# Kernel optimization log

Measured on AMD Instinct MI355X. Metric: run time of the kernel, lower is better.

The kernel has to match this reference:

```python
import jax, jax.numpy as jnp
import numpy as np

NEG = -1e12


def setup_inputs() -> dict:
    key = jax.random.key(0)
    ks = jax.random.split(key, 10)
    B, C, Q, D = 16, 384, 64, 2048
    return {
        "c": jax.random.normal(ks[0], (B, C, D), dtype=jnp.float32),
        "q": jax.random.normal(ks[1], (B, Q, D), dtype=jnp.float32),
        "c_len": jax.random.randint(ks[2], (B,), 1, C + 1),
        "q_len": jax.random.randint(ks[3], (B,), 1, Q + 1),
        "w_c": jax.random.normal(ks[4], (D,), dtype=jnp.float32) * 0.02,
        "b_c": jnp.zeros((), dtype=jnp.float32),
        "w_q": jax.random.normal(ks[5], (D,), dtype=jnp.float32) * 0.02,
        "b_q": jnp.zeros((), dtype=jnp.float32),
        "w_cq": jax.random.normal(ks[6], (D,), dtype=jnp.float32) * 0.02,
        "b_cq": jnp.zeros((), dtype=jnp.float32),
        "W_out": jax.random.normal(ks[7], (4 * D, 2), dtype=jnp.float32) * 0.02,
        "b_out": jnp.zeros((2,), dtype=jnp.float32),
    }


def reference(c, q, c_len, q_len, w_c, b_c, w_q, b_q, w_cq, b_cq, W_out, b_out):
    B, C, D = c.shape
    Q = q.shape[1]
    # trilinear similarity: s[b,r,i] = w_c.c_r + w_q.q_i + w_cq.(c_r*q_i) + biases
    cq = jnp.einsum('bcd,bqd,d->bcq', c, q, w_cq) + b_cq          # [B,C,Q]
    s = (c @ w_c + b_c)[:, :, None] + (q @ w_q + b_q)[:, None, :] + cq
    rows = jnp.arange(C)[None, :, None]
    cols = jnp.arange(Q)[None, None, :]
    # faithful to the triple loop: cols >= q_len OR (rows >= c_len AND col < Q-1)
    masked = (cols >= q_len[:, None, None]) | (
        (rows >= c_len[:, None, None]) & (cols < Q - 1))
    s = s + jnp.where(masked, jnp.float32(NEG), jnp.float32(0.0))
    a = jax.nn.softmax(s, axis=2)                                  # [B,C,Q]
    c2q = jnp.einsum('bcq,bqd->bcd', a, q)                         # [B,C,D]
    b_att = jax.nn.softmax(jnp.max(s, axis=2), axis=1)             # [B,C]
    q2c = jnp.einsum('bc,bcd->bd', b_att, c)[:, None, :]           # [B,1,D]
    x = jnp.concatenate(
        [c, c2q, c * c2q, c * jnp.broadcast_to(q2c, c.shape)], axis=-1)
    out = x @ W_out + b_out                                        # [B,C,2]
    # final masking: out[i][c_len[i]:-1] = NEG (last row untouched)
    row_mask = (jnp.arange(C)[None, :] >= c_len[:, None]) & (
        jnp.arange(C)[None, :] < C - 1)
    out = jnp.where(row_mask[..., None], jnp.float32(NEG), out)
    return out[..., 0], out[..., 1]
```

## Files before the change

### kernel.cpp

```cpp
#include <hip/hip_runtime.h>

#define NEGV -1.0e12f
constexpr int B = 16, C = 384, Q = 64, D = 2048;
constexpr int PITCH = 40;
constexpr int IST = 8320;
constexpr int NIMG = 64;
constexpr int NT = 96;
constexpr int KC = 4;
constexpr int SP = 208;

typedef __attribute__((ext_vector_type(8))) short s16x8;
typedef __attribute__((ext_vector_type(4))) float f32x4;

__device__ __forceinline__ unsigned pkbf(float lo, float hi) {
  unsigned ulo = __builtin_bit_cast(unsigned, lo);
  unsigned uhi = __builtin_bit_cast(unsigned, hi);
  return (uhi & 0xFFFF0000u) | (ulo >> 16);
}
__device__ __forceinline__ float bflo(unsigned u) {
  return __builtin_bit_cast(float, u << 16);
}
__device__ __forceinline__ float bfhi(unsigned u) {
  return __builtin_bit_cast(float, u & 0xFFFF0000u);
}

#define GLD_LDS(gsrc, ldst)                                              \
  __builtin_amdgcn_global_load_lds(                                      \
      (const __attribute__((address_space(1))) unsigned*)(gsrc),         \
      (__attribute__((address_space(3))) unsigned*)(ldst), 16, 0, 0)

__global__ __launch_bounds__(256) void k_pq(
    const float* __restrict__ q, const float* __restrict__ w_cq,
    const float* __restrict__ w_c, const float* __restrict__ w_q,
    const float* __restrict__ W_out, unsigned short* __restrict__ bpk,
    float* __restrict__ qstats) {
  const int t = threadIdx.x;
  if (blockIdx.x < 512) {
    const int s = blockIdx.x & 31, b = blockIdx.x >> 5;
    const int k0 = s * 64;
    unsigned short* base = bpk + (size_t)b * NIMG * IST;
#pragma unroll
    for (int i = 0; i < 4; ++i) {
      int idx = t + 256 * i;
      int qi = idx >> 4, kc = (idx & 15) * 4;
      unsigned short* img = base + (size_t)(s * 2 + (kc >> 5)) * IST;
      const int ko = kc & 31;
      float4 qv = *(const float4*)(q + ((size_t)b * Q + qi) * D + k0 + kc);
      float4 wq = *(const float4*)(w_cq + k0 + kc);
      const float* wp = W_out + (size_t)(2 * D + k0 + kc) * 2;
      float4 wa = *(const float4*)(wp);
      float4 wb = *(const float4*)(wp + 4);
      uint2 u;
      u.x = pkbf(qv.x * wq.x, qv.y * wq.y);
      u.y = pkbf(qv.z * wq.z, qv.w * wq.w);
      *(uint2*)(img + qi * PITCH + ko) = u;
      u.x = pkbf(qv.x * wa.x, qv.y * wa.z);
      u.y = pkbf(qv.z * wb.x, qv.w * wb.z);
      *(uint2*)(img + (64 + qi) * PITCH + ko) = u;
      u.x = pkbf(qv.x * wa.y, qv.y * wa.w);
      u.y = pkbf(qv.z * wb.y, qv.w * wb.w);
      *(uint2*)(img + (128 + qi) * PITCH + ko) = u;
    }
    if (t < 48) {
      int r = t >> 4, kc = (t & 15) * 4;
      unsigned short* img = base + (size_t)(s * 2 + (kc >> 5)) * IST;
      const int ko = kc & 31;
      uint2 u;
      if (r == 0) {
        float4 w = *(const float4*)(w_c + k0 + kc);
        u.x = pkbf(w.x, w.y);
        u.y = pkbf(w.z, w.w);
      } else {
        const float* wp = W_out + (size_t)(k0 + kc) * 2 + (r - 1);
        u.x = pkbf(wp[0], wp[2]);
        u.y = pkbf(wp[4], wp[6]);
      }
      *(uint2*)(img + (192 + r) * PITCH + ko) = u;
    }
  } else {
    int bi = blockIdx.x - 512;
    const float* qrow = q + (size_t)bi * D;
    float a0 = 0.f, a1 = 0.f, a2 = 0.f;
    for (int d = t * 4; d < D; d += 256 * 4) {
      float4 qv = *(const float4*)(qrow + d);
      float4 wq = *(const float4*)(w_q + d);
      const float* wp = W_out + (size_t)(D + d) * 2;
      float4 wa = *(const float4*)(wp);
      float4 wb = *(const float4*)(wp + 4);
      a0 += qv.x * wq.x + qv.y * wq.y + qv.z * wq.z + qv.w * wq.w;
      a1 += qv.x * wa.x + qv.y * wa.z + qv.z * wb.x + qv.w * wb.z;
      a2 += qv.x * wa.y + qv.y * wa.w + qv.z * wb.y + qv.w * wb.w;
    }
    for (int m = 1; m < 64; m <<= 1) {
      a0 += __shfl_xor(a0, m, 64);
      a1 += __shfl_xor(a1, m, 64);
      a2 += __shfl_xor(a2, m, 64);
    }
    __shared__ float red[3][4];
    int w = t >> 6, lane = t & 63;
    if (lane == 0) { red[0][w] = a0; red[1][w] = a1; red[2][w] = a2; }
    __syncthreads();
    if (t == 0) {
      qstats[bi * 3 + 0] = red[0][0] + red[0][1] + red[0][2] + red[0][3];
      qstats[bi * 3 + 1] = red[1][0] + red[1][1] + red[1][2] + red[1][3];
      qstats[bi * 3 + 2] = red[2][0] + red[2][1] + red[2][2] + red[2][3];
    }
  }
}

__global__ __launch_bounds__(512, 2) void k_score(
    const unsigned short* __restrict__ bpk, const float* __restrict__ c,
    float* __restrict__ S3p, unsigned short* __restrict__ cbf) {
  const int t = threadIdx.x;
  const int lane = t & 63, wv = t >> 6;
  const int bid = blockIdx.x;
  const int b = bid & 15, kcb = (bid >> 4) & 3, n0 = (bid >> 6) * NT;
  const int lr = lane & 15, lg = lane >> 4;
  const int mg = wv >> 1, ng = wv & 1;

  __shared__ unsigned short sBp[2][IST];
  __shared__ unsigned short sCp[2][NT * PITCH];

  const unsigned short* gB = bpk + ((size_t)b * NIMG + kcb * 16) * IST;
  const float* cbase = c + ((size_t)b * C + n0) * D + kcb * 512;
  unsigned short* cbf_base = cbf + ((size_t)b * C + n0) * D + kcb * 512;

  f32x4 acc[4][3];
#pragma unroll
  for (int f = 0; f < 4; ++f)
#pragma unroll
    for (int g = 0; g < 3; ++g) acc[f][g] = f32x4{0.f, 0.f, 0.f, 0.f};

  auto stageB = [&](int buf, int s) {
    const char* src = (const char*)gB + (size_t)s * (IST * 2);
    char* dst = (char*)&sBp[buf][0];
    GLD_LDS(src + t * 16, dst + t * 16);
    GLD_LDS(src + 8192 + t * 16, dst + 8192 + t * 16);
    if (t < 16) GLD_LDS(src + 16384 + t * 16, dst + 16384 + t * 16);
  };
  auto loadC = [&](float4* r, int s) {
    const float* base = cbase + s * 32;
    if (wv < 4) {
      int g0 = wv * 128 + lane;
      r[0] = *(const float4*)(base + (size_t)(g0 >> 3) * D + (g0 & 7) * 4);
      int g1 = g0 + 64;
      r[1] = *(const float4*)(base + (size_t)(g1 >> 3) * D + (g1 & 7) * 4);
    } else {
      int g0 = 512 + (wv - 4) * 64 + lane;
      r[0] = *(const float4*)(base + (size_t)(g0 >> 3) * D + (g0 & 7) * 4);
    }
  };
  auto writeC = [&](int buf, const float4* r, int s) {
    unsigned short* cb = cbf_base + s * 32;
    if (wv < 4) {
      int g0 = wv * 128 + lane;
      uint2 u0 = {pkbf(r[0].x, r[0].y), pkbf(r[0].z, r[0].w)};
      *(uint2*)&sCp[buf][(g0 >> 3) * PITCH + (g0 & 7) * 4] = u0;
      *(uint2*)(cb + (size_t)(g0 >> 3) * D + (g0 & 7) * 4) = u0;
      int g1 = g0 + 64;
      uint2 u1 = {pkbf(r[1].x, r[1].y), pkbf(r[1].z, r[1].w)};
      *(uint2*)&sCp[buf][(g1 >> 3) * PITCH + (g1 & 7) * 4] = u1;
      *(uint2*)(cb + (size_t)(g1 >> 3) * D + (g1 & 7) * 4) = u1;
    } else {
      int g0 = 512 + (wv - 4) * 64 + lane;
      uint2 u0 = {pkbf(r[0].x, r[0].y), pkbf(r[0].z, r[0].w)};
      *(uint2*)&sCp[buf][(g0 >> 3) * PITCH + (g0 & 7) * 4] = u0;
      *(uint2*)(cb + (size_t)(g0 >> 3) * D + (g0 & 7) * 4) = u0;
    }
  };
  auto compute = [&](int buf) {
    s16x8 af[4], bf[3];
#pragma unroll
    for (int f = 0; f < 4; ++f)
      af[f] = *(const s16x8*)&sBp[buf][(mg * 64 + f * 16 + lr) * PITCH +
                                       lg * 8];
#pragma unroll
    for (int g = 0; g < 3; ++g)
      bf[g] = *(const s16x8*)&sCp[buf][((ng * 3 + g) * 16 + lr) * PITCH +
                                       lg * 8];
#pragma unroll
    for (int f = 0; f < 4; ++f)
#pragma unroll
      for (int g = 0; g < 3; ++g)
        acc[f][g] =
            __builtin_amdgcn_mfma_f32_16x16x32_bf16(af[f], bf[g], acc[f][g],
                                                    0, 0, 0);
  };

  const int nvm = (wv == 0) ? 5 : ((wv < 4) ? 4 : 3);

  float4 rc[2][2];
  stageB(0, 0);
  loadC(rc[0], 0);
  for (int s = 0; s < 16; ++s) {
    const int cur = s & 1;
    if (s + 1 < 16) {
      stageB(cur ^ 1, s + 1);
      loadC(rc[cur ^ 1], s + 1);
      if (nvm == 5)
        asm volatile("s_waitcnt vmcnt(5)" ::: "memory");
      else if (nvm == 4)
        asm volatile("s_waitcnt vmcnt(4)" ::: "memory");
      else
        asm volatile("s_waitcnt vmcnt(3)" ::: "memory");
    } else {
      asm volatile("s_waitcnt vmcnt(0)" ::: "memory");
    }
    writeC(cur, rc[cur], s);
    asm volatile("s_waitcnt lgkmcnt(0)" ::: "memory");
    __builtin_amdgcn_sched_barrier(0);
    __builtin_amdgcn_s_barrier();
    compute(cur);
    __builtin_amdgcn_s_barrier();
  }

  const size_t rowbase = ((size_t)kcb * B + b) * C;
#pragma unroll
  for (int f = 0; f < 4; ++f) {
    int mf = mg * 4 + f;
    if (mf < 13) {
#pragma unroll
      for (int g = 0; g < 3; ++g) {
        int n = n0 + (ng * 3 + g) * 16 + lr;
        float* p = S3p + (rowbase + n) * SP + mf * 16 + lg * 4;
        *(f32x4*)p = acc[f][g];
      }
    }
  }
}

__global__ __launch_bounds__(256) void k_soft(
    const float* __restrict__ S3p, const float* __restrict__ qstats,
    const int* __restrict__ c_len, const int* __restrict__ q_len,
    const float* __restrict__ b_c, const float* __restrict__ b_q,
    const float* __restrict__ b_cq, float* __restrict__ mrow,
    float* __restrict__ out12) {
  const int t = threadIdx.x, lane = t & 63;
  const int rg = blockIdx.x * 4 + (t >> 6);
  const int b = rg / C, r = rg % C;
  float s_cq = 0.f, sc = 0.f, w10 = 0.f, w11 = 0.f, t30 = 0.f, t31 = 0.f;
#pragma unroll
  for (int p = 0; p < KC; ++p) {
    const float* Sr = S3p + ((size_t)p * B * C + rg) * SP;
    s_cq += Sr[lane];
    sc += Sr[192];
    w10 += Sr[193];
    w11 += Sr[194];
    t30 += Sr[64 + lane];
    t31 += Sr[128 + lane];
  }
  const float qs0 = qstats[((b << 6) + lane) * 3 + 0];
  const float qs1 = qstats[((b << 6) + lane) * 3 + 1];
  const float qs2 = qstats[((b << 6) + lane) * 3 + 2];
  float s = s_cq + sc + qs0 + b_c[0] + b_q[0] + b_cq[0];
  const int cl = c_len[b], ql = q_len[b];
  bool masked = (lane >= ql) || ((r >= cl) && (lane < Q - 1));
  if (masked) s += NEGV;
  float mx = s;
  for (int m = 1; m < 64; m <<= 1) mx = fmaxf(mx, __shfl_xor(mx, m, 64));
  float e = __expf(s - mx);
  float den = e;
  for (int m = 1; m < 64; m <<= 1) den += __shfl_xor(den, m, 64);
  float a = e / den;
  float v0 = a * (qs1 + t30);
  float v1 = a * (qs2 + t31);
  for (int m = 1; m < 64; m <<= 1) {
    v0 += __shfl_xor(v0, m, 64);
    v1 += __shfl_xor(v1, m, 64);
  }
  if (lane == 0) {
    mrow[rg] = mx;
    out12[rg * 2 + 0] = w10 + v0;
    out12[rg * 2 + 1] = w11 + v1;
  }
}

__global__ __launch_bounds__(512) void k_q2cu(
    const unsigned short* __restrict__ cbf, const float* __restrict__ mrow,
    const float* __restrict__ W_out, float* __restrict__ uvec) {
  const int ch = blockIdx.x, b = blockIdx.y;
  const int t = threadIdx.x, lane = t & 63, wv = t >> 6;
  __shared__ float batt[C];
  __shared__ float rmx[8], rsm[8];
  __shared__ float redq0[8][64], redq1[8][64];

  float m = (t < C) ? mrow[b * C + t] : -3.0e38f;
  float mx = m;
  for (int o = 1; o < 64; o <<= 1) mx = fmaxf(mx, __shfl_xor(mx, o, 64));
  if (lane == 0) rmx[wv] = mx;
  __syncthreads();
  mx = rmx[0];
#pragma unroll
  for (int i = 1; i < 8; ++i) mx = fmaxf(mx, rmx[i]);
  float e = (t < C) ? __expf(m - mx) : 0.f;
  float sm = e;
  for (int o = 1; o < 64; o <<= 1) sm += __shfl_xor(sm, o, 64);
  if (lane == 0) rsm[wv] = sm;
  __syncthreads();
  sm = rsm[0] + rsm[1] + rsm[2] + rsm[3] + rsm[4] + rsm[5] + rsm[6] + rsm[7];
  if (t < C) batt[t] = e / sm;
  __syncthreads();

  const int d0 = ch * 128 + lane * 2;
  const unsigned short* p = cbf + ((size_t)b * C + wv * 8) * D + d0;
  float A0[8] = {0.f, 0.f, 0.f, 0.f, 0.f, 0.f, 0.f, 0.f};
  float A1[8] = {0.f, 0.f, 0.f, 0.f, 0.f, 0.f, 0.f, 0.f};
#pragma unroll
  for (int r0 = 0; r0 < 384; r0 += 64) {
    const unsigned short* pr = p + (size_t)r0 * D;
    const float* bt = &batt[r0 + wv * 8];
#pragma unroll
    for (int j = 0; j < 8; ++j) {
      unsigned cc = *(const unsigned*)(pr + (size_t)j * D);
      A0[j] += bt[j] * bflo(cc);
      A1[j] += bt[j] * bfhi(cc);
    }
  }
  float s0 = ((A0[0] + A0[1]) + (A0[2] + A0[3])) +
             ((A0[4] + A0[5]) + (A0[6] + A0[7]));
  float s1 = ((A1[0] + A1[1]) + (A1[2] + A1[3])) +
             ((A1[4] + A1[5]) + (A1[6] + A1[7]));
  redq0[wv][lane] = s0;
  redq1[wv][lane] = s1;
  __syncthreads();
  if (t < 64) {
    float q0 = 0.f, q1 = 0.f;
#pragma unroll
    for (int w = 0; w < 8; ++w) {
      q0 += redq0[w][t];
      q1 += redq1[w][t];
    }
    int dd = ch * 128 + t * 2;
    float4 w4 = *(const float4*)(W_out + (size_t)(3 * D + dd) * 2);
    float4 u = {q0 * w4.x, q0 * w4.y, q1 * w4.z, q1 * w4.w};
    *(float4*)(uvec + ((size_t)b * D + dd) * 2) = u;
  }
}

__global__ __launch_bounds__(512) void k_out(
    const unsigned short* __restrict__ cbf, const float* __restrict__ uvec,
    const float* __restrict__ out12, const float* __restrict__ b_out,
    const int* __restrict__ c_len, float* __restrict__ outp) {
  const int b = blockIdx.y, r0 = blockIdx.x * 8;
  const int t = threadIdx.x, lane = t & 63, wv = t >> 6;
  __shared__ float u_sh[2 * D];

  {
    const float* src = uvec + (size_t)b * D * 2 + t * 8;
    float4 v0 = *(const float4*)(src);
    float4 v1 = *(const float4*)(src + 4);
    *(float4*)&u_sh[t * 8] = v0;
    *(float4*)&u_sh[t * 8 + 4] = v1;
  }
  __syncthreads();

  const int r = r0 + wv;
  const unsigned short* crow = cbf + ((size_t)b * C + r) * D;
  float o0 = 0.f, o1 = 0.f;
#pragma unroll
  for (int it = 0; it < 16; ++it) {
    int d0 = it * 128 + lane * 2;
    unsigned cc = *(const unsigned*)(crow + d0);
    float c0 = bflo(cc), c1 = bfhi(cc);
    float4 u = *(const float4*)&u_sh[d0 * 2];
    o0 += c0 * u.x + c1 * u.z;
    o1 += c0 * u.y + c1 * u.w;
  }
  for (int o = 1; o < 64; o <<= 1) {
    o0 += __shfl_xor(o0, o, 64);
    o1 += __shfl_xor(o1, o, 64);
  }
  if (lane == 0) {
    const int idx = b * C + r;
    o0 += out12[idx * 2 + 0] + b_out[0];
    o1 += out12[idx * 2 + 1] + b_out[1];
    if (r >= c_len[b] && r < C - 1) { o0 = NEGV; o1 = NEGV; }
    outp[idx] = o0;
    outp[B * C + idx] = o1;
  }
}

extern "C" void kernel_launch(void* const* d_in, const int* in_sizes, int n_in,
                              void* d_out, int out_size, void* d_ws,
                              size_t ws_size, hipStream_t stream) {
  const float* c = (const float*)d_in[0];
  const float* q = (const float*)d_in[1];
  const int* c_len = (const int*)d_in[2];
  const int* q_len = (const int*)d_in[3];
  const float* w_c = (const float*)d_in[4];
  const float* b_c = (const float*)d_in[5];
  const float* w_q = (const float*)d_in[6];
  const float* b_q = (const float*)d_in[7];
  const float* w_cq = (const float*)d_in[8];
  const float* b_cq = (const float*)d_in[9];
  const float* W_out = (const float*)d_in[10];
  const float* b_out = (const float*)d_in[11];
  float* outp = (float*)d_out;

  unsigned short* bpk = (unsigned short*)d_ws;
  const size_t bpk_bytes = (size_t)B * NIMG * IST * 2;
  float* S3p = (float*)((char*)d_ws + bpk_bytes);
  const size_t s3_elems = (size_t)KC * B * C * SP;
  float* ws = S3p + s3_elems;
  float* qstats = ws;
  float* mrow = ws + 3072;
  float* out12 = ws + 3072 + 6144;
  float* uvec = ws + 3072 + 6144 + 12288;
  unsigned short* cbf = (unsigned short*)(uvec + 65536);

  hipLaunchKernelGGL(k_pq, dim3(512 + B * Q), dim3(256), 0, stream, q, w_cq,
                     w_c, w_q, W_out, bpk, qstats);
  hipLaunchKernelGGL(k_score, dim3(4 * KC * B), dim3(512), 0, stream, bpk, c,
                     S3p, cbf);
  hipLaunchKernelGGL(k_soft, dim3(B * C / 4), dim3(256), 0, stream, S3p,
                     qstats, c_len, q_len, b_c, b_q, b_cq, mrow, out12);
  hipLaunchKernelGGL(k_q2cu, dim3(16, B), dim3(512), 0, stream, cbf, mrow,
                     W_out, uvec);
  hipLaunchKernelGGL(k_out, dim3(C / 8, B), dim3(512), 0, stream, cbf, uvec,
                     out12, b_out, c_len, outp);
}
```

Before: 49.18 us.

## Triple-buffer k_score loads and store split-K partial scores as bf16

The k_score main loop moves from double to triple buffering: stages are prefetched two steps ahead, with per-wave vmcnt waits adjusted to match. This needs about 1.5x the LDS, so launch bounds drop to one block per CU. The split-K partial score buffer S3p is now written and read as bf16 instead of fp32, halving that intermediate traffic between k_score and k_soft. The cost is lower occupancy and precision lost on partial sums before softmax, which could exceed tolerance.

```diff
diff --git a/kernel.cpp b/kernel.cpp
--- a/kernel.cpp
+++ b/kernel.cpp
@@ -22,6 +22,9 @@
 }
 __device__ __forceinline__ float bfhi(unsigned u) {
   return __builtin_bit_cast(float, u & 0xFFFF0000u);
+}
+__device__ __forceinline__ float bfs(unsigned short u) {
+  return __builtin_bit_cast(float, ((unsigned)u) << 16);
 }
 
 #define GLD_LDS(gsrc, ldst)                                              \
@@ -108,9 +111,9 @@
   }
 }
 
-__global__ __launch_bounds__(512, 2) void k_score(
+__global__ __launch_bounds__(512, 1) void k_score(
     const unsigned short* __restrict__ bpk, const float* __restrict__ c,
-    float* __restrict__ S3p, unsigned short* __restrict__ cbf) {
+    unsigned short* __restrict__ S3pb, unsigned short* __restrict__ cbf) {
   const int t = threadIdx.x;
   const int lane = t & 63, wv = t >> 6;
   const int bid = blockIdx.x;
@@ -118,8 +121,8 @@
   const int lr = lane & 15, lg = lane >> 4;
   const int mg = wv >> 1, ng = wv & 1;
 
-  __shared__ unsigned short sBp[2][IST];
-  __shared__ unsigned short sCp[2][NT * PITCH];
+  __shared__ unsigned short sBp[3][IST];
+  __shared__ unsigned short sCp[3][NT * PITCH];
 
   const unsigned short* gB = bpk + ((size_t)b * NIMG + kcb * 16) * IST;
   const float* cbase = c + ((size_t)b * C + n0) * D + kcb * 512;
@@ -187,22 +190,37 @@
                                                     0, 0, 0);
   };
 
-  const int nvm = (wv == 0) ? 5 : ((wv < 4) ? 4 : 3);
-
-  float4 rc[2][2];
+  auto vmwait2 = [&]() {
+    if (wv == 0)
+      asm volatile("s_waitcnt vmcnt(14)" ::: "memory");
+    else if (wv < 4)
+      asm volatile("s_waitcnt vmcnt(12)" ::: "memory");
+    else
+      asm volatile("s_waitcnt vmcnt(8)" ::: "memory");
+  };
+  auto vmwait1 = [&]() {
+    if (wv == 0)
+      asm volatile("s_waitcnt vmcnt(7)" ::: "memory");
+    else if (wv < 4)
+      asm volatile("s_waitcnt vmcnt(6)" ::: "memory");
+    else
+      asm volatile("s_waitcnt vmcnt(4)" ::: "memory");
+  };
+
+  float4 rc[3][2];
   stageB(0, 0);
   loadC(rc[0], 0);
+  stageB(1, 1);
+  loadC(rc[1], 1);
+#pragma unroll
   for (int s = 0; s < 16; ++s) {
-    const int cur = s & 1;
-    if (s + 1 < 16) {
-      stageB(cur ^ 1, s + 1);
-      loadC(rc[cur ^ 1], s + 1);
-      if (nvm == 5)
-        asm volatile("s_waitcnt vmcnt(5)" ::: "memory");
-      else if (nvm == 4)
-        asm volatile("s_waitcnt vmcnt(4)" ::: "memory");
-      else
-        asm volatile("s_waitcnt vmcnt(3)" ::: "memory");
+    const int cur = s % 3;
+    if (s + 2 < 16) {
+      stageB((s + 2) % 3, s + 2);
+      loadC(rc[(s + 2) % 3], s + 2);
+      vmwait2();
+    } else if (s + 1 < 16) {
+      vmwait1();
     } else {
       asm volatile("s_waitcnt vmcnt(0)" ::: "memory");
     }
@@ -222,15 +240,17 @@
 #pragma unroll
       for (int g = 0; g < 3; ++g) {
         int n = n0 + (ng * 3 + g) * 16 + lr;
-        float* p = S3p + (rowbase + n) * SP + mf * 16 + lg * 4;
-        *(f32x4*)p = acc[f][g];
+        uint2 pk;
+        pk.x = pkbf(acc[f][g][0], acc[f][g][1]);
+        pk.y = pkbf(acc[f][g][2], acc[f][g][3]);
+        *(uint2*)(S3pb + (rowbase + n) * SP + mf * 16 + lg * 4) = pk;
       }
     }
   }
 }
 
 __global__ __launch_bounds__(256) void k_soft(
-    const float* __restrict__ S3p, const float* __restrict__ qstats,
+    const unsigned short* __restrict__ S3pb, const float* __restrict__ qstats,
     const int* __restrict__ c_len, const int* __restrict__ q_len,
     const float* __restrict__ b_c, const float* __restrict__ b_q,
     const float* __restrict__ b_cq, float* __restrict__ mrow,
@@ -241,13 +261,13 @@
   float s_cq = 0.f, sc = 0.f, w10 = 0.f, w11 = 0.f, t30 = 0.f, t31 = 0.f;
 #pragma unroll
   for (int p = 0; p < KC; ++p) {
-    const float* Sr = S3p + ((size_t)p * B * C + rg) * SP;
-    s_cq += Sr[lane];
-    sc += Sr[192];
-    w10 += Sr[193];
-    w11 += Sr[194];
-    t30 += Sr[64 + lane];
-    t31 += Sr[128 + lane];
+    const unsigned short* Sr = S3pb + ((size_t)p * B * C + rg) * SP;
+    s_cq += bfs(Sr[lane]);
+    sc += bfs(Sr[192]);
+    w10 += bfs(Sr[193]);
+    w11 += bfs(Sr[194]);
+    t30 += bfs(Sr[64 + lane]);
+    t31 += bfs(Sr[128 + lane]);
   }
   const float qs0 = qstats[((b << 6) + lane) * 3 + 0];
   const float qs1 = qstats[((b << 6) + lane) * 3 + 1];
@@ -399,9 +419,9 @@
 
   unsigned short* bpk = (unsigned short*)d_ws;
   const size_t bpk_bytes = (size_t)B * NIMG * IST * 2;
-  float* S3p = (float*)((char*)d_ws + bpk_bytes);
+  unsigned short* S3pb = (unsigned short*)((char*)d_ws + bpk_bytes);
   const size_t s3_elems = (size_t)KC * B * C * SP;
-  float* ws = S3p + s3_elems;
+  float* ws = (float*)(S3pb + s3_elems);
   float* qstats = ws;
   float* mrow = ws + 3072;
   float* out12 = ws + 3072 + 6144;
@@ -411,8 +431,8 @@
   hipLaunchKernelGGL(k_pq, dim3(512 + B * Q), dim3(256), 0, stream, q, w_cq,
                      w_c, w_q, W_out, bpk, qstats);
   hipLaunchKernelGGL(k_score, dim3(4 * KC * B), dim3(512), 0, stream, bpk, c,
-                     S3p, cbf);
-  hipLaunchKernelGGL(k_soft, dim3(B * C / 4), dim3(256), 0, stream, S3p,
+                     S3pb, cbf);
+  hipLaunchKernelGGL(k_soft, dim3(B * C / 4), dim3(256), 0, stream, S3pb,
                      qstats, c_len, q_len, b_c, b_q, b_cq, mrow, out12);
   hipLaunchKernelGGL(k_q2cu, dim3(16, B), dim3(512), 0, stream, cbf, mrow,
                      W_out, uvec);
```

After: 47.91 us. -2.6%, faster.
